# Kernel tuning notes

Hardware: AMD Instinct MI355X
Metric: run time of the kernel (lower is better)

Reference implementation:

```python
import jax, jax.numpy as jnp
import numpy as np

IN_FEAT = 10
HID = 32
B, N = 256, 512


def setup_inputs() -> dict:
    key = jax.random.key(0)
    k1, k2, k3, k4 = jax.random.split(key, 4)
    s = jax.random.normal(k1, (B, N, IN_FEAT), dtype=jnp.float32)
    Gmat = jax.random.uniform(k2, (B, N, N), dtype=jnp.float32)
    # match torch init: rand * (4/in)**0.5 - (1/in)**0.5
    scale = (4.0 / IN_FEAT) ** 0.5
    shift = (1.0 / IN_FEAT) ** 0.5
    Qweight = jax.random.uniform(k3, (IN_FEAT, HID), dtype=jnp.float32) * scale - shift
    Kweight = jax.random.uniform(k4, (IN_FEAT, HID), dtype=jnp.float32) * scale - shift
    return {"s": s, "Gmat": Gmat, "Qweight": Qweight, "Kweight": Kweight}


def reference(s, Gmat, Qweight, Kweight):
    q = jnp.einsum('bnk,km->bnm', s, Qweight)          # [B, N, HID]
    k = jnp.einsum('bnk,km->bnm', s, Kweight)          # [B, N, HID]
    scores = jnp.einsum('bnm,bjm->bnj', q, k)          # [B, N, N] = q @ k^T
    att = jnp.square(scores) * Gmat
    att = att / (jnp.sum(att, axis=2, keepdims=True) + 0.001)
    return att
```

## Files before the change

kernel.cpp:

```cpp
#include <hip/hip_runtime.h>

#define BB 256
#define NN 512
#define FF 10
#define HH 32


#define PASS_BODY(J0, SC)                                                     \
    do {                                                                      \
        __syncthreads();     \
        {                                                                     \
            const int m  = t & 31;                                            \
            const int jg = t >> 5;                                  \
            for (int i = 0; i < 32; ++i) {                                    \
                const int j = jg * 32 + i;                  \
                float acc = 0.f;                                              \
                _Pragma("unroll")                                             \
                for (int f = 0; f < FF; ++f)                                  \
                    acc += s_lds[((J0) + j) * FF + f] * kw_lds[f * HH + m];   \
                k_lds[j * 36 + m] = acc;                                      \
            }                                                                 \
        }                                                                     \
        __syncthreads();                                                      \
        _Pragma("unroll")                                                     \
        for (int mc = 0; mc < 8; ++mc) {                                      \
            float4 kf[4];                                                     \
            _Pragma("unroll")                                                 \
            for (int c = 0; c < 4; ++c)                                       \
                kf[c] = *(const float4*)&k_lds[(lane + 64 * c) * 36 + mc * 4];\
            _Pragma("unroll")                                                 \
            for (int r = 0; r < 8; ++r) {                                     \
                const float4 q4 =                                             \
                    *(const float4*)&q_lds[(r0 + r) * 36 + mc * 4];           \
                _Pragma("unroll")                                             \
                for (int c = 0; c < 4; ++c) {                                 \
                    SC[r][c] += q4.x * kf[c].x + q4.y * kf[c].y               \
                              + q4.z * kf[c].z + q4.w * kf[c].w;              \
                }                                                             \
            }                                                                 \
        }                                                                     \
    } while (0)

__global__ __launch_bounds__(256, 2)
void att_kernel(const float* __restrict__ s,
                const float* __restrict__ G,
                const float* __restrict__ Qw,
                const float* __restrict__ Kw,
                float* __restrict__ out) {
    __shared__ float s_lds[NN * FF];
    __shared__ float k_lds[256 * 36];
    __shared__ float q_lds[32 * 36];
    __shared__ float qw_lds[FF * HH];
    __shared__ float kw_lds[FF * HH];

    const int t    = threadIdx.x;
    const int b    = blockIdx.x >> 4;
    const int tile = blockIdx.x & 15;
    const int row0 = tile * 32;
    const int wave = t >> 6;
    const int lane = t & 63;
    const int r0   = wave * 8;

    float g[8][8];
    const float* Gb = G + (size_t)b * NN * NN;
    #pragma unroll
    for (int r = 0; r < 8; ++r) {
        const float* gp = Gb + (size_t)(row0 + r0 + r) * NN + lane;
        #pragma unroll
        for (int c = 0; c < 8; ++c) g[r][c] = gp[64 * c];
    }

    const float* sb = s + (size_t)b * NN * FF;
    for (int i = t; i < NN * FF; i += 256) s_lds[i] = sb[i];
    for (int i = t; i < FF * HH; i += 256) { qw_lds[i] = Qw[i]; kw_lds[i] = Kw[i]; }
    __syncthreads();

    {
        const int m = t & 31;
        const int rg = t >> 5;
        #pragma unroll
        for (int rr = 0; rr < 4; ++rr) {
            const int rl = rg + 8 * rr;
            float acc = 0.f;
            #pragma unroll
            for (int f = 0; f < FF; ++f)
                acc += s_lds[(row0 + rl) * FF + f] * qw_lds[f * HH + m];
            q_lds[rl * 36 + m] = acc;
        }
    }

    float scA[8][4], scB[8][4];
    #pragma unroll
    for (int r = 0; r < 8; ++r)
        #pragma unroll
        for (int c = 0; c < 4; ++c) { scA[r][c] = 0.f; scB[r][c] = 0.f; }

    PASS_BODY(0,   scA);
    PASS_BODY(256, scB);

    float* ob = out + (size_t)b * NN * NN;
    #pragma unroll
    for (int r = 0; r < 8; ++r) {
        float a[8];
        float rs = 0.f;
        #pragma unroll
        for (int c = 0; c < 4; ++c) {
            float v = scA[r][c];
            v = v * v * g[r][c];
            a[c] = v;
            rs += v;
        }
        #pragma unroll
        for (int c = 0; c < 4; ++c) {
            float v = scB[r][c];
            v = v * v * g[r][4 + c];
            a[4 + c] = v;
            rs += v;
        }
        #pragma unroll
        for (int off = 32; off > 0; off >>= 1) rs += __shfl_xor(rs, off, 64);
        const float inv = 1.0f / (rs + 0.001f);
        float* op = ob + (size_t)(row0 + r0 + r) * NN + lane;
        #pragma unroll
        for (int c = 0; c < 8; ++c) op[64 * c] = a[c] * inv;
    }
}

extern "C" void kernel_launch(void* const* d_in, const int* in_sizes, int n_in,
                              void* d_out, int out_size, void* d_ws, size_t ws_size,
                              hipStream_t stream) {
    const float* s  = (const float*)d_in[0];
    const float* G  = (const float*)d_in[1];
    const float* Qw = (const float*)d_in[2];
    const float* Kw = (const float*)d_in[3];
    float* out = (float*)d_out;
    dim3 grid(BB * 16);
    dim3 block(256);
    att_kernel<<<grid, block, 0, stream>>>(s, G, Qw, Kw, out);
}
```

Before: 503.7 us.

## Fold Q and K weights into a 10x10 matrix and drop per-block K projection

Scores are now computed as s_i·(Qw Kwᵀ)·s_jᵀ. The kernel builds a 10x10 matrix M once per block and a 32x10 row transform, so the HID-dimension dot products are gone, as are the two K-projection passes and their syncs. s is stored transposed in LDS so each lane can pull its column features directly. The block grows to 512 threads with 4 rows per wave, and G is loaded at the epilogue instead of being prefetched into registers up front. The trade-off is less latency hiding for the G read and a slightly different float summation order.

```diff
diff --git a/kernel.cpp b/kernel.cpp
--- a/kernel.cpp
+++ b/kernel.cpp
@@ -6,50 +6,40 @@
 #define HH 32
 
 
-#define PASS_BODY(J0, SC)                                                     \
+#define HALF_BODY(CC, SC)                                                     \
     do {                                                                      \
-        __syncthreads();     \
-        {                                                                     \
-            const int m  = t & 31;                                            \
-            const int jg = t >> 5;                                  \
-            for (int i = 0; i < 32; ++i) {                                    \
-                const int j = jg * 32 + i;                  \
-                float acc = 0.f;                                              \
-                _Pragma("unroll")                                             \
-                for (int f = 0; f < FF; ++f)                                  \
-                    acc += s_lds[((J0) + j) * FF + f] * kw_lds[f * HH + m];   \
-                k_lds[j * 36 + m] = acc;                                      \
-            }                                                                 \
+        float sj[4][FF];                                                      \
+        _Pragma("unroll")                                                     \
+        for (int c4 = 0; c4 < 4; ++c4) {                                      \
+            const int j = lane + 64 * ((CC) * 4 + c4);                        \
+            _Pragma("unroll")                                                 \
+            for (int f = 0; f < FF; ++f) sj[c4][f] = st_lds[f][j];            \
         }                                                                     \
-        __syncthreads();                                                      \
         _Pragma("unroll")                                                     \
-        for (int mc = 0; mc < 8; ++mc) {                                      \
-            float4 kf[4];                                                     \
+        for (int r = 0; r < 4; ++r) {                                         \
+            const float4 t0 = *(const float4*)&t_lds[r0 + r][0];              \
+            const float4 t1 = *(const float4*)&t_lds[r0 + r][4];              \
+            const float2 t2 = *(const float2*)&t_lds[r0 + r][8];              \
             _Pragma("unroll")                                                 \
-            for (int c = 0; c < 4; ++c)                                       \
-                kf[c] = *(const float4*)&k_lds[(lane + 64 * c) * 36 + mc * 4];\
-            _Pragma("unroll")                                                 \
-            for (int r = 0; r < 8; ++r) {                                     \
-                const float4 q4 =                                             \
-                    *(const float4*)&q_lds[(r0 + r) * 36 + mc * 4];           \
-                _Pragma("unroll")                                             \
-                for (int c = 0; c < 4; ++c) {                                 \
-                    SC[r][c] += q4.x * kf[c].x + q4.y * kf[c].y               \
-                              + q4.z * kf[c].z + q4.w * kf[c].w;              \
-                }                                                             \
+            for (int c4 = 0; c4 < 4; ++c4) {                                  \
+                SC[r][c4] += t0.x * sj[c4][0] + t0.y * sj[c4][1]              \
+                           + t0.z * sj[c4][2] + t0.w * sj[c4][3]              \
+                           + t1.x * sj[c4][4] + t1.y * sj[c4][5]              \
+                           + t1.z * sj[c4][6] + t1.w * sj[c4][7]              \
+                           + t2.x * sj[c4][8] + t2.y * sj[c4][9];             \
             }                                                                 \
         }                                                                     \
     } while (0)
 
-__global__ __launch_bounds__(256, 2)
+__global__ __launch_bounds__(512, 4)
 void att_kernel(const float* __restrict__ s,
                 const float* __restrict__ G,
                 const float* __restrict__ Qw,
                 const float* __restrict__ Kw,
                 float* __restrict__ out) {
-    __shared__ float s_lds[NN * FF];
-    __shared__ float k_lds[256 * 36];
-    __shared__ float q_lds[32 * 36];
+    __shared__ float st_lds[FF][NN];
+    __shared__ float t_lds[32][12];
+    __shared__ float m_lds[FF][FF];
     __shared__ float qw_lds[FF * HH];
     __shared__ float kw_lds[FF * HH];
 
@@ -59,70 +49,73 @@
     const int row0 = tile * 32;
     const int wave = t >> 6;
     const int lane = t & 63;
-    const int r0   = wave * 8;
-
-    float g[8][8];
-    const float* Gb = G + (size_t)b * NN * NN;
-    #pragma unroll
-    for (int r = 0; r < 8; ++r) {
-        const float* gp = Gb + (size_t)(row0 + r0 + r) * NN + lane;
-        #pragma unroll
-        for (int c = 0; c < 8; ++c) g[r][c] = gp[64 * c];
-    }
+    const int r0   = wave * 4;
 
     const float* sb = s + (size_t)b * NN * FF;
-    for (int i = t; i < NN * FF; i += 256) s_lds[i] = sb[i];
-    for (int i = t; i < FF * HH; i += 256) { qw_lds[i] = Qw[i]; kw_lds[i] = Kw[i]; }
+    for (int i = t; i < NN * FF; i += 512) {
+        const int j = i / FF, f = i % FF;
+        st_lds[f][j] = sb[i];
+    }
+    if (t < FF * HH) { qw_lds[t] = Qw[t]; kw_lds[t] = Kw[t]; }
     __syncthreads();
 
-    {
-        const int m = t & 31;
-        const int rg = t >> 5;
+    if (t < FF * FF) {
+        const int f = t / FF, f2 = t % FF;
+        float acc = 0.f;
         #pragma unroll
-        for (int rr = 0; rr < 4; ++rr) {
-            const int rl = rg + 8 * rr;
-            float acc = 0.f;
-            #pragma unroll
-            for (int f = 0; f < FF; ++f)
-                acc += s_lds[(row0 + rl) * FF + f] * qw_lds[f * HH + m];
-            q_lds[rl * 36 + m] = acc;
-        }
+        for (int m = 0; m < HH; ++m)
+            acc += qw_lds[f * HH + m] * kw_lds[f2 * HH + m];
+        m_lds[f][f2] = acc;
     }
+    __syncthreads();
 
-    float scA[8][4], scB[8][4];
+    if (t < 32 * FF) {
+        const int rl = t / FF, f2 = t % FF;
+        float acc = 0.f;
+        #pragma unroll
+        for (int f = 0; f < FF; ++f)
+            acc += st_lds[f][row0 + rl] * m_lds[f][f2];
+        t_lds[rl][f2] = acc;
+    }
+    __syncthreads();
+
+    float scA[4][4], scB[4][4];
     #pragma unroll
-    for (int r = 0; r < 8; ++r)
+    for (int r = 0; r < 4; ++r)
         #pragma unroll
         for (int c = 0; c < 4; ++c) { scA[r][c] = 0.f; scB[r][c] = 0.f; }
 
-    PASS_BODY(0,   scA);
-    PASS_BODY(256, scB);
+    HALF_BODY(0, scA);
+    HALF_BODY(1, scB);
 
+    const float* Gb = G + (size_t)b * NN * NN;
     float* ob = out + (size_t)b * NN * NN;
     #pragma unroll
-    for (int r = 0; r < 8; ++r) {
+    for (int r = 0; r < 4; ++r) {
+        const size_t rowoff = (size_t)(row0 + r0 + r) * NN + lane;
+        const float* gp = Gb + rowoff;
         float a[8];
         float rs = 0.f;
         #pragma unroll
         for (int c = 0; c < 4; ++c) {
             float v = scA[r][c];
-            v = v * v * g[r][c];
-            a[c] = v;
-            rs += v;
+            v = v * v * gp[64 * c];
+            a[c] = v; rs += v;
         }
         #pragma unroll
         for (int c = 0; c < 4; ++c) {
             float v = scB[r][c];
-            v = v * v * g[r][4 + c];
-            a[4 + c] = v;
-            rs += v;
+            v = v * v * gp[256 + 64 * c];
+            a[4 + c] = v; rs += v;
         }
         #pragma unroll
         for (int off = 32; off > 0; off >>= 1) rs += __shfl_xor(rs, off, 64);
         const float inv = 1.0f / (rs + 0.001f);
-        float* op = ob + (size_t)(row0 + r0 + r) * NN + lane;
+        float* op = ob + rowoff;
         #pragma unroll
-        for (int c = 0; c < 8; ++c) op[64 * c] = a[c] * inv;
+        for (int c = 0; c < 4; ++c) op[64 * c] = a[c] * inv;
+        #pragma unroll
+        for (int c = 0; c < 4; ++c) op[256 + 64 * c] = a[4 + c] * inv;
     }
 }
 
@@ -135,6 +128,6 @@
     const float* Kw = (const float*)d_in[3];
     float* out = (float*)d_out;
     dim3 grid(BB * 16);
-    dim3 block(256);
+    dim3 block(512);
     att_kernel<<<grid, block, 0, stream>>>(s, G, Qw, Kw, out);
 }
```

Result: faster. 472.3 us (-6.2%).
